# Kernel tuning notes

Measured on AMD Instinct MI355X. Metric: run time of the kernel, lower is better.

## Reference

```python
import jax, jax.numpy as jnp
import numpy as np

BATCH, SEQ, D_IN = 4, 2048, 1024
STATE, D_OUT, KX = 1024, 1024, 10


def setup_inputs() -> dict:
    key = jax.random.key(0)
    k0, k1, k2, k3, k4, k5 = jax.random.split(key, 6)
    inputs = jax.random.normal(k0, (BATCH, SEQ, D_IN), jnp.float32)
    h0 = jax.random.normal(k1, (STATE,), jnp.float32)
    A = jax.random.normal(k2, (STATE,), jnp.float32)
    A = A / jnp.max(jnp.abs(A))  # matches init_A / max|init_A|
    B = jax.random.normal(k3, (D_IN, STATE), jnp.float32) / D_IN
    C = jax.random.normal(k4, (STATE, D_OUT), jnp.float32) / STATE
    M = jax.random.normal(k5, (D_IN, D_OUT, KX), jnp.float32) / D_OUT
    return {"inputs": inputs, "h0": h0, "A": A, "B": B, "C": C, "M": M}


def compute_ar_x_preds(w, x):
    # w: (d_out, d_in, k); x: (b, l, d_in)
    d_out, d_in, k = w.shape
    b, l, _ = x.shape
    o = jnp.einsum('oik,bli->bklo', w, x)  # (b, k, l, d_out)
    shifts = jnp.arange(k)
    # roll slice i forward by i along the length axis
    o = jax.vmap(lambda oi, s: jnp.roll(oi, s, axis=1), in_axes=(1, 0), out_axes=1)(o, shifts)
    # triu mask: keep position t in slice i only if t >= i (causal AR)
    m = (jnp.arange(l)[None, :] >= shifts[:, None]).astype(o.dtype)  # (k, l)
    return jnp.sum(o * m[None, :, :, None], axis=1)  # (b, l, d_out)


def reference(inputs, h0, A, B, C, M):
    bsz = inputs.shape[0]
    h_init = jnp.broadcast_to(h0, (bsz, h0.shape[0]))  # h0.expand(bsz, state_dim)
    u_seq = jnp.swapaxes(inputs, 0, 1)  # (l, b, d_in)

    def step(h, u):
        h_new = A * h + u @ B  # diagonal recurrence
        return h_new, h_new

    _, hs = jax.lax.scan(step, h_init, u_seq)  # (l, b, state)
    all_h_t = jnp.swapaxes(hs, 0, 1)  # (b, l, state)
    lds_out = all_h_t @ C  # (b, l, d_out)
    ar = compute_ar_x_preds(M, inputs)
    return lds_out + ar
```

## Files before the change

### kernel.cpp

```cpp
#include <hip/hip_runtime.h>
#include <stdint.h>

typedef unsigned short u16;
typedef __attribute__((ext_vector_type(4))) float f32x4;
typedef __attribute__((ext_vector_type(8))) short s16x8;

#define BATCH 4
#define SEQ   2048
#define DIM   1024
#define KX    10
#define PAD   16
#define SEQP  (SEQ+PAD)

__device__ __forceinline__ u16 f2b(float f) {
    union { float f; uint32_t u; } v; v.f = f;
    uint32_t u = v.u + 0x7fffu + ((v.u >> 16) & 1u);
    return (u16)(u >> 16);
}
__device__ __forceinline__ float b2f(u16 h) {
    union { uint32_t u; float f; } v; v.u = ((uint32_t)h) << 16;
    return v.f;
}

__device__ __forceinline__ void llds16(const u16* g, u16* l) {
    __builtin_amdgcn_global_load_lds(
        (const __attribute__((address_space(1))) uint32_t*)g,
        (__attribute__((address_space(3))) uint32_t*)l, 16, 0, 0);
}

#define PREP_X_END  8256
#define PREP_C_END  10304
#define PREP_M_END  14400

__global__ __launch_bounds__(256) void k_prep(
    const float* __restrict__ x, const float* __restrict__ B,
    const float* __restrict__ C, const float* __restrict__ M,
    u16* __restrict__ Xpad, u16* __restrict__ Btr, u16* __restrict__ Wall)
{
    __shared__ float tile[32][33];
    const int bid = blockIdx.x, tid = threadIdx.x;

    if (bid < PREP_X_END) {
        int idx = bid * 256 + tid;
        long e = (long)idx * 4;
        int i = (int)(e & 1023);
        int row = (int)(e >> 10);
        int t = row % SEQP;
        int b = row / SEQP;
        ushort4 o;
        if (t < PAD) {
            o.x = 0; o.y = 0; o.z = 0; o.w = 0;
        } else {
            const float4 v = *(const float4*)(x + (((long)(b * SEQ + (t - PAD)) << 10) + i));
            o.x = f2b(v.x); o.y = f2b(v.y); o.z = f2b(v.z); o.w = f2b(v.w);
        }
        *(ushort4*)(Xpad + ((long)row << 10) + i) = o;
    } else if (bid < PREP_C_END) {
        const int tb = bid - PREP_X_END;
        const float* in = (tb < 1024) ? B : C;
        u16* out = (tb < 1024) ? Btr : Wall;
        int lb = tb & 1023;
        int bx = lb & 31, by = lb >> 5;
        int tx = tid & 31, ty = tid >> 5;
#pragma unroll
        for (int j = 0; j < 4; j++)
            tile[ty + j * 8][tx] = in[(long)(by * 32 + ty + j * 8) * 1024 + bx * 32 + tx];
        __syncthreads();
#pragma unroll
        for (int j = 0; j < 4; j++)
            out[(long)(bx * 32 + ty + j * 8) * 1024 + by * 32 + tx] = f2b(tile[tx][ty + j * 8]);
    } else {
        int idx = (bid - PREP_C_END) * 256 + tid;
        int o = idx >> 10, i = idx & 1023;
        const float* src = M + (long)idx * KX;
#pragma unroll
        for (int k = 0; k < KX; k++)
            Wall[((long)(k + 1) << 20) + ((long)o << 10) + i] = f2b(src[k]);
    }
}


__global__ void k_scan1(const u16* __restrict__ U, const float* __restrict__ A,
                        float* __restrict__ F) {
    int s = blockIdx.x * 256 + threadIdx.x;
    int bc = blockIdx.y;
    int b = bc >> 4, c = bc & 15;
    float a = A[s];
    const u16* u = U + (((long)(b * SEQ + c * 128)) << 10) + s;
    float f = 0.f;
#pragma unroll 8
    for (int j = 0; j < 128; j++) f = fmaf(a, f, b2f(u[(long)j << 10]));
    F[((long)bc << 10) + s] = f;
}

__global__ void k_scan2(const float* __restrict__ F, const float* __restrict__ A,
                        const float* __restrict__ h0, float* __restrict__ Carry) {
    int idx = blockIdx.x * 256 + threadIdx.x;
    int b = idx >> 10, s = idx & 1023;
    float a = A[s];
    float a128 = a;
#pragma unroll
    for (int q = 0; q < 7; q++) a128 *= a128;
    float carry = h0[s];
#pragma unroll
    for (int c = 0; c < 16; c++) {
        long off = ((long)(b * 16 + c) << 10) + s;
        Carry[off] = carry;
        carry = fmaf(a128, carry, F[off]);
    }
}

__global__ void k_scan3(u16* __restrict__ U, const float* __restrict__ A,
                        const float* __restrict__ Carry) {
    int s = blockIdx.x * 256 + threadIdx.x;
    int bc = blockIdx.y;
    int b = bc >> 4, c = bc & 15;
    float a = A[s];
    long base = (((long)(b * SEQ + c * 128)) << 10) + s;
    float h = Carry[((long)bc << 10) + s];
#pragma unroll 8
    for (int j = 0; j < 128; j++) {
        h = fmaf(a, h, b2f(U[base + ((long)j << 10)]));
        U[base + ((long)j << 10)] = f2b(h);
    }
}

__global__ __launch_bounds__(128) void k_gemm(
    void* __restrict__ outv, const u16* __restrict__ Xpad,
    const u16* __restrict__ Hbf, const u16* __restrict__ W,
    int ngroups, int use_h, int bf16_out)
{
    __shared__ u16 Asl[160 * 64];
    __shared__ u16 Wb2[2][64 * 64];

    const int tid  = threadIdx.x;
    const int wave = tid >> 6, lane = tid & 63;
    const int quad = lane >> 4, l15 = lane & 15, l7 = lane & 7;

    const int col0 = blockIdx.x * 64;
    const int row0 = blockIdx.y * 128;
    const int bb = row0 >> 11;
    const long Xrow0 = (long)bb * SEQP + PAD + (row0 & (SEQ - 1));
    const long XslabBase = (Xrow0 - 16) << 10;
    const int lastg = ngroups - 1;

    f32x4 acc[4][4];
#pragma unroll
    for (int i = 0; i < 4; i++)
#pragma unroll
        for (int j = 0; j < 4; j++)
            acc[i][j] = (f32x4){0.f, 0.f, 0.f, 0.f};

    for (int k0 = 0; k0 < 1024; k0 += 64) {
#pragma unroll
        for (int q = 0; q < 10; q++) {
            int u = wave * 640 + q * 64 + lane;
            int row = u >> 3;
            int kc = (u & 7) ^ (row & 7);
            llds16(Xpad + XslabBase + ((long)row << 10) + k0 + kc * 8,
                   &Asl[(wave * 640 + q * 64) * 8]);
        }
        {
            int wsel = use_h ? 1 : 0;
            const u16* Wg = W + ((long)wsel << 20) + ((long)col0 << 10);
#pragma unroll
            for (int q = 0; q < 4; q++) {
                int u = wave * 256 + q * 64 + lane;
                int row = u >> 3;
                int kc = (u & 7) ^ (row & 7);
                llds16(Wg + ((long)row << 10) + k0 + kc * 8,
                       &Wb2[0][(wave * 256 + q * 64) * 8]);
            }
        }
        __syncthreads();

        for (int g = 0; g < ngroups; g++) {
            const bool isH = use_h && (g == lastg);
            if (isH) {
                const u16* Hb = Hbf + ((long)row0 << 10);
#pragma unroll
                for (int q = 0; q < 8; q++) {
                    int u = wave * 512 + q * 64 + lane;
                    int row = u >> 3;
                    int kc = (u & 7) ^ (row & 7);
                    llds16(Hb + ((long)row << 10) + k0 + kc * 8,
                           &Asl[(wave * 512 + q * 64) * 8]);
                }
                __syncthreads();
            }
            if (g < lastg) {
                int gn = g + 1;
                int wsel = use_h ? ((gn == lastg) ? 0 : gn + 1) : gn;
                const u16* Wg = W + ((long)wsel << 20) + ((long)col0 << 10);
                u16* dst = Wb2[gn & 1];
#pragma unroll
                for (int q = 0; q < 4; q++) {
                    int u = wave * 256 + q * 64 + lane;
                    int row = u >> 3;
                    int kc = (u & 7) ^ (row & 7);
                    llds16(Wg + ((long)row << 10) + k0 + kc * 8,
                           &dst[(wave * 256 + q * 64) * 8]);
                }
            }

            const int rbase = isH ? 0 : (16 - g);
            const int r7 = (l15 + rbase) & 7;
            const u16* Wrd = Wb2[g & 1];

            s16x8 af[4][2], bfr[4][2];
#pragma unroll
            for (int mi = 0; mi < 4; mi++) {
                int arow = rbase + wave * 64 + mi * 16 + l15;
#pragma unroll
                for (int kk = 0; kk < 2; kk++) {
                    int kca = ((kk * 4 + quad) ^ r7) << 3;
                    int kcb = ((kk * 4 + quad) ^ l7) << 3;
                    af[mi][kk]  = *(const s16x8*)&Asl[arow * 64 + kca];
                    bfr[mi][kk] = *(const s16x8*)&Wrd[(mi * 16 + l15) * 64 + kcb];
                }
            }
#pragma unroll
            for (int mi = 0; mi < 4; mi++)
#pragma unroll
                for (int ni = 0; ni < 4; ni++) {
                    acc[mi][ni] = __builtin_amdgcn_mfma_f32_16x16x32_bf16(
                        af[mi][0], bfr[ni][0], acc[mi][ni], 0, 0, 0);
                    acc[mi][ni] = __builtin_amdgcn_mfma_f32_16x16x32_bf16(
                        af[mi][1], bfr[ni][1], acc[mi][ni], 0, 0, 0);
                }
            __syncthreads();
        }
    }

#pragma unroll
    for (int mi = 0; mi < 4; mi++) {
        int r = row0 + wave * 64 + mi * 16 + quad * 4;
#pragma unroll
        for (int ni = 0; ni < 4; ni++) {
            int c = col0 + ni * 16 + l15;
            f32x4 v = acc[mi][ni];
            if (bf16_out) {
                u16* ob = (u16*)outv;
#pragma unroll
                for (int reg = 0; reg < 4; reg++)
                    ob[((long)(r + reg) << 10) + c] = f2b(v[reg]);
            } else {
                float* of = (float*)outv;
#pragma unroll
                for (int reg = 0; reg < 4; reg++)
                    of[((long)(r + reg) << 10) + c] = v[reg];
            }
        }
    }
}


extern "C" void kernel_launch(void* const* d_in, const int* in_sizes, int n_in,
                              void* d_out, int out_size, void* d_ws, size_t ws_size,
                              hipStream_t stream) {
    const float* x  = (const float*)d_in[0];
    const float* h0 = (const float*)d_in[1];
    const float* A  = (const float*)d_in[2];
    const float* B  = (const float*)d_in[3];
    const float* C  = (const float*)d_in[4];
    const float* M  = (const float*)d_in[5];
    float* out = (float*)d_out;

    char* ws = (char*)d_ws;
    u16*   Xpad  = (u16*)  (ws);
    u16*   Wall  = (u16*)  (ws + 16908288);
    u16*   Btr   = (u16*)  (ws + 39976960);
    u16*   Ubf   = (u16*)  (ws + 42074112);
    float* F     = (float*)(ws + 58851328);
    float* Carry = (float*)(ws + 59113472);

    k_prep<<<dim3(PREP_M_END), dim3(256), 0, stream>>>(x, B, C, M, Xpad, Btr, Wall);

    k_gemm<<<dim3(16, 64), dim3(128), 0, stream>>>(Ubf, Xpad, Ubf, Btr, 1, 0, 1);

    k_scan1<<<dim3(4, 64), dim3(256), 0, stream>>>(Ubf, A, F);
    k_scan2<<<dim3(16), dim3(256), 0, stream>>>(F, A, h0, Carry);
    k_scan3<<<dim3(4, 64), dim3(256), 0, stream>>>(Ubf, A, Carry);

    k_gemm<<<dim3(16, 64), dim3(128), 0, stream>>>(out, Xpad, Ubf, Wall, 11, 1, 0);
}
```

Measured before the change: 335.4 us.

## Split GEMM K dimension across two wave pairs with LDS reduction

The GEMM block grows from 2 to 4 waves. The two wave pairs each handle half of the K range (0-511 and 512-1023) over 32-wide k-steps, and the partial accumulators are summed through shared memory before the store. The aim is more waves per block to hide latency and raise MFMA issue without changing the output tile. The cost is twice as many k-iterations and barriers per block, narrower 32-wide LDS slabs with a 4-way swizzle, and an extra LDS reduction in the epilogue.

```diff
diff --git a/kernel.cpp b/kernel.cpp
--- a/kernel.cpp
+++ b/kernel.cpp
@@ -125,17 +125,17 @@
     }
 }
 
-__global__ __launch_bounds__(128) void k_gemm(
+__global__ __launch_bounds__(256, 4) void k_gemm(
     void* __restrict__ outv, const u16* __restrict__ Xpad,
     const u16* __restrict__ Hbf, const u16* __restrict__ W,
     int ngroups, int use_h, int bf16_out)
 {
-    __shared__ u16 Asl[160 * 64];
-    __shared__ u16 Wb2[2][64 * 64];
+    __shared__ u16 smem[18432];
 
     const int tid  = threadIdx.x;
     const int wave = tid >> 6, lane = tid & 63;
-    const int quad = lane >> 4, l15 = lane & 15, l7 = lane & 7;
+    const int pair = wave >> 1, wm = wave & 1;
+    const int quad = lane >> 4, l15 = lane & 15;
 
     const int col0 = blockIdx.x * 64;
     const int row0 = blockIdx.y * 128;
@@ -151,104 +151,141 @@
         for (int j = 0; j < 4; j++)
             acc[i][j] = (f32x4){0.f, 0.f, 0.f, 0.f};
 
-    for (int k0 = 0; k0 < 1024; k0 += 64) {
-#pragma unroll
-        for (int q = 0; q < 10; q++) {
-            int u = wave * 640 + q * 64 + lane;
-            int row = u >> 3;
-            int kc = (u & 7) ^ (row & 7);
-            llds16(Xpad + XslabBase + ((long)row << 10) + k0 + kc * 8,
-                   &Asl[(wave * 640 + q * 64) * 8]);
-        }
-        {
-            int wsel = use_h ? 1 : 0;
-            const u16* Wg = W + ((long)wsel << 20) + ((long)col0 << 10);
-#pragma unroll
-            for (int q = 0; q < 4; q++) {
-                int u = wave * 256 + q * 64 + lane;
-                int row = u >> 3;
-                int kc = (u & 7) ^ (row & 7);
-                llds16(Wg + ((long)row << 10) + k0 + kc * 8,
-                       &Wb2[0][(wave * 256 + q * 64) * 8]);
-            }
-        }
+    auto stageX2 = [&](int k0) {
+#pragma unroll
+        for (int p = 0; p < 2; p++) {
+            const int kb = k0 + p * 512;
+            u16* slab = smem + p * 5120;
+#pragma unroll
+            for (int q = 0; q < 2; q++) {
+                int u = q * 256 + tid;
+                int row = u >> 2;
+                int kc = (u & 3) ^ (row & 3);
+                llds16(Xpad + XslabBase + ((long)row << 10) + kb + kc * 8,
+                       &slab[(q * 256 + wave * 64) * 8]);
+            }
+            {
+                int u = 512 + tid;
+                int row = u >> 2;
+                int kc = (u & 3) ^ (row & 3);
+                if (tid < 128)
+                    llds16(Xpad + XslabBase + ((long)row << 10) + kb + kc * 8,
+                           &slab[(512 + wave * 64) * 8]);
+            }
+        }
+    };
+    auto stageW2 = [&](int k0, int wsel, int parity) {
+        const u16* Wg = W + ((long)wsel << 20) + ((long)col0 << 10);
+#pragma unroll
+        for (int p = 0; p < 2; p++) {
+            int row = tid >> 2;
+            int kc = (tid & 3) ^ (row & 3);
+            llds16(Wg + ((long)row << 10) + (k0 + p * 512) + kc * 8,
+                   &smem[10240 + (p * 2 + parity) * 2048 + wave * 64 * 8]);
+        }
+    };
+    auto stageH2 = [&](int k0) {
+        const u16* Hb = Hbf + ((long)row0 << 10);
+#pragma unroll
+        for (int p = 0; p < 2; p++) {
+            const int kb = k0 + p * 512;
+            u16* slab = smem + p * 5120;
+#pragma unroll
+            for (int q = 0; q < 2; q++) {
+                int u = q * 256 + tid;
+                int row = u >> 2;
+                int kc = (u & 3) ^ (row & 3);
+                llds16(Hb + ((long)row << 10) + kb + kc * 8,
+                       &slab[(q * 256 + wave * 64) * 8]);
+            }
+        }
+    };
+
+    const u16* slab  = smem + pair * 5120;
+    const u16* Wpair = smem + 10240 + pair * 2 * 2048;
+
+    for (int k0 = 0; k0 < 512; k0 += 32) {
+        stageX2(k0);
+        stageW2(k0, use_h ? 1 : 0, 0);
         __syncthreads();
 
         for (int g = 0; g < ngroups; g++) {
             const bool isH = use_h && (g == lastg);
             if (isH) {
-                const u16* Hb = Hbf + ((long)row0 << 10);
-#pragma unroll
-                for (int q = 0; q < 8; q++) {
-                    int u = wave * 512 + q * 64 + lane;
-                    int row = u >> 3;
-                    int kc = (u & 7) ^ (row & 7);
-                    llds16(Hb + ((long)row << 10) + k0 + kc * 8,
-                           &Asl[(wave * 512 + q * 64) * 8]);
-                }
+                stageH2(k0);
                 __syncthreads();
             }
             if (g < lastg) {
                 int gn = g + 1;
                 int wsel = use_h ? ((gn == lastg) ? 0 : gn + 1) : gn;
-                const u16* Wg = W + ((long)wsel << 20) + ((long)col0 << 10);
-                u16* dst = Wb2[gn & 1];
-#pragma unroll
-                for (int q = 0; q < 4; q++) {
-                    int u = wave * 256 + q * 64 + lane;
-                    int row = u >> 3;
-                    int kc = (u & 7) ^ (row & 7);
-                    llds16(Wg + ((long)row << 10) + k0 + kc * 8,
-                           &dst[(wave * 256 + q * 64) * 8]);
+                stageW2(k0, wsel, gn & 1);
+            }
+
+            const int rbase = isH ? 0 : (16 - g);
+            const u16* Wrd = Wpair + (g & 1) * 2048;
+
+            s16x8 af[4], bfr[4];
+#pragma unroll
+            for (int mi = 0; mi < 4; mi++) {
+                int arow = rbase + wm * 64 + mi * 16 + l15;
+                int kca = (quad ^ (arow & 3)) << 3;
+                af[mi] = *(const s16x8*)&slab[arow * 32 + kca];
+            }
+#pragma unroll
+            for (int ni = 0; ni < 4; ni++) {
+                int brow = ni * 16 + l15;
+                int kcb = (quad ^ (brow & 3)) << 3;
+                bfr[ni] = *(const s16x8*)&Wrd[brow * 32 + kcb];
+            }
+#pragma unroll
+            for (int mi = 0; mi < 4; mi++)
+#pragma unroll
+                for (int ni = 0; ni < 4; ni++)
+                    acc[mi][ni] = __builtin_amdgcn_mfma_f32_16x16x32_bf16(
+                        af[mi], bfr[ni], acc[mi][ni], 0, 0, 0);
+            __syncthreads();
+        }
+    }
+
+    float* scr = (float*)smem;
+    if (pair == 1) {
+#pragma unroll
+        for (int mi = 0; mi < 4; mi++) {
+            int rl = wm * 64 + mi * 16 + quad * 4;
+#pragma unroll
+            for (int ni = 0; ni < 4; ni++) {
+                int c = ni * 16 + l15;
+                f32x4 v = acc[mi][ni];
+#pragma unroll
+                for (int reg = 0; reg < 4; reg++)
+                    scr[(rl + reg) * 64 + c] = v[reg];
+            }
+        }
+    }
+    __syncthreads();
+    if (pair == 0) {
+#pragma unroll
+        for (int mi = 0; mi < 4; mi++) {
+            int rl = wm * 64 + mi * 16 + quad * 4;
+            int r = row0 + rl;
+#pragma unroll
+            for (int ni = 0; ni < 4; ni++) {
+                int cl = ni * 16 + l15;
+                int c = col0 + cl;
+                f32x4 v = acc[mi][ni];
+                if (bf16_out) {
+                    u16* ob = (u16*)outv;
+#pragma unroll
+                    for (int reg = 0; reg < 4; reg++)
+                        ob[((long)(r + reg) << 10) + c] =
+                            f2b(v[reg] + scr[(rl + reg) * 64 + cl]);
+                } else {
+                    float* of = (float*)outv;
+#pragma unroll
+                    for (int reg = 0; reg < 4; reg++)
+                        of[((long)(r + reg) << 10) + c] =
+                            v[reg] + scr[(rl + reg) * 64 + cl];
                 }
-            }
-
-            const int rbase = isH ? 0 : (16 - g);
-            const int r7 = (l15 + rbase) & 7;
-            const u16* Wrd = Wb2[g & 1];
-
-            s16x8 af[4][2], bfr[4][2];
-#pragma unroll
-            for (int mi = 0; mi < 4; mi++) {
-                int arow = rbase + wave * 64 + mi * 16 + l15;
-#pragma unroll
-                for (int kk = 0; kk < 2; kk++) {
-                    int kca = ((kk * 4 + quad) ^ r7) << 3;
-                    int kcb = ((kk * 4 + quad) ^ l7) << 3;
-                    af[mi][kk]  = *(const s16x8*)&Asl[arow * 64 + kca];
-                    bfr[mi][kk] = *(const s16x8*)&Wrd[(mi * 16 + l15) * 64 + kcb];
-                }
-            }
-#pragma unroll
-            for (int mi = 0; mi < 4; mi++)
-#pragma unroll
-                for (int ni = 0; ni < 4; ni++) {
-                    acc[mi][ni] = __builtin_amdgcn_mfma_f32_16x16x32_bf16(
-                        af[mi][0], bfr[ni][0], acc[mi][ni], 0, 0, 0);
-                    acc[mi][ni] = __builtin_amdgcn_mfma_f32_16x16x32_bf16(
-                        af[mi][1], bfr[ni][1], acc[mi][ni], 0, 0, 0);
-                }
-            __syncthreads();
-        }
-    }
-
-#pragma unroll
-    for (int mi = 0; mi < 4; mi++) {
-        int r = row0 + wave * 64 + mi * 16 + quad * 4;
-#pragma unroll
-        for (int ni = 0; ni < 4; ni++) {
-            int c = col0 + ni * 16 + l15;
-            f32x4 v = acc[mi][ni];
-            if (bf16_out) {
-                u16* ob = (u16*)outv;
-#pragma unroll
-                for (int reg = 0; reg < 4; reg++)
-                    ob[((long)(r + reg) << 10) + c] = f2b(v[reg]);
-            } else {
-                float* of = (float*)outv;
-#pragma unroll
-                for (int reg = 0; reg < 4; reg++)
-                    of[((long)(r + reg) << 10) + c] = v[reg];
             }
         }
     }
@@ -276,11 +313,11 @@
 
     k_prep<<<dim3(PREP_M_END), dim3(256), 0, stream>>>(x, B, C, M, Xpad, Btr, Wall);
 
-    k_gemm<<<dim3(16, 64), dim3(128), 0, stream>>>(Ubf, Xpad, Ubf, Btr, 1, 0, 1);
+    k_gemm<<<dim3(16, 64), dim3(256), 0, stream>>>(Ubf, Xpad, Ubf, Btr, 1, 0, 1);
 
     k_scan1<<<dim3(4, 64), dim3(256), 0, stream>>>(Ubf, A, F);
     k_scan2<<<dim3(16), dim3(256), 0, stream>>>(F, A, h0, Carry);
     k_scan3<<<dim3(4, 64), dim3(256), 0, stream>>>(Ubf, A, Carry);
 
-    k_gemm<<<dim3(16, 64), dim3(128), 0, stream>>>(out, Xpad, Ubf, Wall, 11, 1, 0);
-}
+    k_gemm<<<dim3(16, 64), dim3(256), 0, stream>>>(out, Xpad, Ubf, Wall, 11, 1, 0);
+}
```

After: 357.1 us. +6.5%, slower.
